# Kernel tuning notes

Hardware: AMD Instinct MI355X
Metric: run time of the kernel (lower is better)

The kernel has to match this reference:

```python
import jax, jax.numpy as jnp
import numpy as np

UP = 4  # upsample factor of DispUpsampleBySlantedPlane


def _l1_warp_cost(fea_l, fea_r, disp):
    """Warp fea_r horizontally by disp (grid_sample bilinear, zeros padding,
    align_corners=True) and return per-pixel L1 distance over channels.
    fea_l, fea_r: [B, C, H, W]; disp: [B, H, W] -> returns [B, H, W]."""
    B, C, H, W = fea_l.shape
    x = jnp.arange(W, dtype=disp.dtype)
    xf = x[None, None, :] - disp              # sample position in right image
    x0 = jnp.floor(xf)
    w1 = xf - x0                              # weight for x0+1
    w0 = 1.0 - w1
    x0i = x0.astype(jnp.int32)
    x1i = x0i + 1
    v0 = ((x0i >= 0) & (x0i < W)).astype(fea_l.dtype)  # zeros padding masks
    v1 = ((x1i >= 0) & (x1i < W)).astype(fea_l.dtype)
    x0c = jnp.clip(x0i, 0, W - 1)
    x1c = jnp.clip(x1i, 0, W - 1)
    idx0 = jnp.broadcast_to(x0c[:, None, :, :], (B, C, H, W))
    idx1 = jnp.broadcast_to(x1c[:, None, :, :], (B, C, H, W))
    g0 = jnp.take_along_axis(fea_r, idx0, axis=3)
    g1 = jnp.take_along_axis(fea_r, idx1, axis=3)
    warped = g0 * (w0 * v0)[:, None] + g1 * (w1 * v1)[:, None]
    return jnp.sum(jnp.abs(fea_l - warped), axis=1)  # L1 over channels


def _tile_warping(tile_plane, fea_l, fea_r):
    B, C, H, W = fea_l.shape
    h, w = tile_plane.shape[2], tile_plane.shape[3]
    d = tile_plane[:, 0]   # [B, h, w]
    dx = tile_plane[:, 1]
    dy = tile_plane[:, 2]
    # slanted-plane offsets for the 4x4 sub-pixels, centered at (UP-1)/2 = 1.5
    off = jnp.arange(UP, dtype=fea_l.dtype) - (UP - 1) / 2.0
    outs = []
    for disp_d in (-1.0, 0.0, 1.0):
        # disp0[b, di, dj, th, tw] = (d + disp_d) + off[di]*dy + off[dj]*dx
        disp0 = ((d + disp_d)[:, None, None]
                 + off[None, :, None, None, None] * dy[:, None, None]
                 + off[None, None, :, None, None] * dx[:, None, None])
        # PixelShuffle(4): full-res disparity [B, H, W]
        disp_full = disp0.transpose(0, 3, 1, 4, 2).reshape(B, H, W)
        cv = _l1_warp_cost(fea_l, fea_r, disp_full)        # [B, H, W]
        # cv[:, :, i::4, j::4] for i,j in 0..3, concatenated on channel dim
        local = cv.reshape(B, h, UP, w, UP).transpose(0, 2, 4, 1, 3)
        outs.append(local.reshape(B, UP * UP, h, w))       # [B, 16, h, w]
    return jnp.concatenate(outs, axis=1)                   # [B, 48, h, w]


def setup_inputs() -> dict:
    key = jax.random.key(0)
    k1, k2, k3 = jax.random.split(key, 3)
    B, C, H, W = 4, 16, 512, 960
    h, w = H // UP, W // UP
    tile_plane = jax.random.normal(k1, (B, 3, h, w), dtype=jnp.float32)
    fea_l = jax.random.normal(k2, (B, C, H, W), dtype=jnp.float32)
    fea_r = jax.random.normal(k3, (B, C, H, W), dtype=jnp.float32)
    return {"tile_plane": tile_plane, "fea_l": fea_l, "fea_r": fea_r}


def reference(tile_plane, fea_l, fea_r):
    return _tile_warping(tile_plane, fea_l, fea_r)
```

## Files before the change

### kernel.cpp

```cpp
#include <hip/hip_runtime.h>


#define NB 4
#define NC 16
#define NH 512
#define NW 960
#define TH 128
#define TW 240
#define HW (NH * NW)
#define SEG 256
#define GUARD 16
#define WIN (SEG + 2 * GUARD)
#define SLOTS (NC * WIN / 4)
#define SLOTS_PER_CH (WIN / 4)

typedef const __attribute__((address_space(1))) unsigned int* gas_u32;
typedef __attribute__((address_space(3))) unsigned int* las_u32;

__device__ __forceinline__ void stage16(const float* g, float* l) {
    __builtin_amdgcn_global_load_lds((gas_u32)g, (las_u32)l, 16, 0, 0);
}

__global__ __launch_bounds__(256, 8) void tile_warp_kernel(
    const float* __restrict__ tp,
    const float* __restrict__ fl,
    const float* __restrict__ fr,
    float* __restrict__ out)
{
    const int t = threadIdx.x;
    const int s = blockIdx.x;
    const int Y = blockIdx.y;
    const int b = blockIdx.z;
    const int base = s * SEG;
    const int X = base + t;

    __shared__ float lds[NC * WIN];

    const float* frrow = fr + (size_t)(b * NC) * HW + (size_t)Y * NW;

#pragma unroll
    for (int k = 0; k < 4; ++k) {
        const int slot = t + 256 * k;
        const int c = slot / SLOTS_PER_CH;
        const int off = slot - c * SLOTS_PER_CH;
        int gx = base - GUARD + 4 * off;
        gx = min(max(gx, 0), NW - 4);
        stage16(frrow + (size_t)c * HW + gx, &lds[4 * slot]);
    }
    if (t < SLOTS - 1024) {
        const int slot = t + 1024;
        const int c = slot / SLOTS_PER_CH;
        const int off = slot - c * SLOTS_PER_CH;
        int gx = base - GUARD + 4 * off;
        gx = min(max(gx, 0), NW - 4);
        stage16(frrow + (size_t)c * HW + gx, &lds[4 * slot]);
    }

    const int y = Y >> 2, i = Y & 3;
    const int j = X & 3;
    const int T = X >> 2;
    const int Tc = min(T, TW - 1);

    const int tpb = (b * 3 * TH + y) * TW + Tc;
    const float d   = tp[tpb];
    const float dxv = tp[tpb + TH * TW];
    const float dyv = tp[tpb + 2 * TH * TW];
    const float disp = d + ((float)i - 1.5f) * dyv + ((float)j - 1.5f) * dxv;
    const float xf  = (float)X - disp;
    const float x0f = floorf(xf);
    const float w1  = xf - x0f;
    const float w0  = 1.0f - w1;
    const int   x0  = (int)x0f;
    const int   p   = x0 - 1;
    const int   q   = p - base + GUARD;
    const int   qc  = min(max(q, 0), WIN - 4);
    const bool  spill = (q != qc) && (X < NW);

    float w0k[3], w1k[3];
#pragma unroll
    for (int kk = 0; kk < 3; ++kk) {
        const int xa = p + 2 - kk;
        const int xb = xa + 1;
        w0k[kk] = (xa >= 0 && xa < NW) ? w0 : 0.0f;
        w1k[kk] = (xb >= 0 && xb < NW) ? w1 : 0.0f;
    }

    const float* flp = fl + (size_t)(b * NC) * HW + (size_t)Y * NW + min(X, NW - 1);

    __syncthreads();

    float a0 = 0.f, a1 = 0.f, a2 = 0.f;
#pragma unroll
    for (int g = 0; g < 4; ++g) {
        float flv[4];
#pragma unroll
        for (int cc = 0; cc < 4; ++cc) flv[cc] = flp[(size_t)(4 * g + cc) * HW];
#pragma unroll
        for (int cc = 0; cc < 4; ++cc) {
            const float* L = &lds[(4 * g + cc) * WIN + qc];
            const float m0 = L[0], m1 = L[1], m2 = L[2], m3 = L[3];
            a0 += fabsf(flv[cc] - (m2 * w0k[0] + m3 * w1k[0]));
            a1 += fabsf(flv[cc] - (m1 * w0k[1] + m2 * w1k[1]));
            a2 += fabsf(flv[cc] - (m0 * w0k[2] + m1 * w1k[2]));
        }
    }

    if (__builtin_expect(spill, 0)) {
        a0 = a1 = a2 = 0.f;
        const int t0 = min(max(p,     0), NW - 1);
        const int t1 = min(max(p + 1, 0), NW - 1);
        const int t2 = min(max(p + 2, 0), NW - 1);
        const int t3 = min(max(p + 3, 0), NW - 1);
        for (int c = 0; c < NC; ++c) {
            const float* R = frrow + (size_t)c * HW;
            const float m0 = R[t0], m1 = R[t1], m2 = R[t2], m3 = R[t3];
            const float fv = flp[(size_t)c * HW];
            a0 += fabsf(fv - (m2 * w0k[0] + m3 * w1k[0]));
            a1 += fabsf(fv - (m1 * w0k[1] + m2 * w1k[1]));
            a2 += fabsf(fv - (m0 * w0k[2] + m1 * w1k[2]));
        }
    }

    if (X < NW) {
        const size_t ob = ((size_t)(b * 48 + i * 4 + j) * TH + y) * TW + T;
        out[ob]                        = a0;
        out[ob + 16 * (size_t)TH * TW] = a1;
        out[ob + 32 * (size_t)TH * TW] = a2;
    }
}

extern "C" void kernel_launch(void* const* d_in, const int* in_sizes, int n_in,
                              void* d_out, int out_size, void* d_ws, size_t ws_size,
                              hipStream_t stream) {
    const float* tp = (const float*)d_in[0];
    const float* fl = (const float*)d_in[1];
    const float* fr = (const float*)d_in[2];
    float* out = (float*)d_out;

    dim3 grid(4, NH, NB);
    dim3 block(256);
    tile_warp_kernel<<<grid, block, 0, stream>>>(tp, fl, fr, out);
}
```

Baseline: 274.2 us.

## Drop LDS staging of right features and gather directly from global memory

Removes the global_load_lds staging of a guarded right-feature window into shared memory, the barrier and the spill fallback path. Each thread now gathers its four right-feature taps per channel straight from global memory and relies on the cache. Blocks grow to 320 threads across 3 segments so the width of 960 divides evenly and the bounds checks go away. This trades LDS traffic and synchronisation for more global load instructions, with locality left to the L1/L2 caches.

```diff
diff --git a/kernel.cpp b/kernel.cpp
--- a/kernel.cpp
+++ b/kernel.cpp
@@ -8,20 +8,8 @@
 #define TH 128
 #define TW 240
 #define HW (NH * NW)
-#define SEG 256
-#define GUARD 16
-#define WIN (SEG + 2 * GUARD)
-#define SLOTS (NC * WIN / 4)
-#define SLOTS_PER_CH (WIN / 4)
 
-typedef const __attribute__((address_space(1))) unsigned int* gas_u32;
-typedef __attribute__((address_space(3))) unsigned int* las_u32;
-
-__device__ __forceinline__ void stage16(const float* g, float* l) {
-    __builtin_amdgcn_global_load_lds((gas_u32)g, (las_u32)l, 16, 0, 0);
-}
-
-__global__ __launch_bounds__(256, 8) void tile_warp_kernel(
+__global__ __launch_bounds__(320) void tile_warp_kernel(
     const float* __restrict__ tp,
     const float* __restrict__ fl,
     const float* __restrict__ fr,
@@ -31,37 +19,11 @@
     const int s = blockIdx.x;
     const int Y = blockIdx.y;
     const int b = blockIdx.z;
-    const int base = s * SEG;
-    const int X = base + t;
+    const int X = s * 320 + t;
+    const int y = Y >> 2, i = Y & 3;
+    const int j = X & 3, T = X >> 2;
 
-    __shared__ float lds[NC * WIN];
-
-    const float* frrow = fr + (size_t)(b * NC) * HW + (size_t)Y * NW;
-
-#pragma unroll
-    for (int k = 0; k < 4; ++k) {
-        const int slot = t + 256 * k;
-        const int c = slot / SLOTS_PER_CH;
-        const int off = slot - c * SLOTS_PER_CH;
-        int gx = base - GUARD + 4 * off;
-        gx = min(max(gx, 0), NW - 4);
-        stage16(frrow + (size_t)c * HW + gx, &lds[4 * slot]);
-    }
-    if (t < SLOTS - 1024) {
-        const int slot = t + 1024;
-        const int c = slot / SLOTS_PER_CH;
-        const int off = slot - c * SLOTS_PER_CH;
-        int gx = base - GUARD + 4 * off;
-        gx = min(max(gx, 0), NW - 4);
-        stage16(frrow + (size_t)c * HW + gx, &lds[4 * slot]);
-    }
-
-    const int y = Y >> 2, i = Y & 3;
-    const int j = X & 3;
-    const int T = X >> 2;
-    const int Tc = min(T, TW - 1);
-
-    const int tpb = (b * 3 * TH + y) * TW + Tc;
+    const int tpb = (b * 3 * TH + y) * TW + T;
     const float d   = tp[tpb];
     const float dxv = tp[tpb + TH * TW];
     const float dyv = tp[tpb + 2 * TH * TW];
@@ -70,11 +32,12 @@
     const float x0f = floorf(xf);
     const float w1  = xf - x0f;
     const float w0  = 1.0f - w1;
-    const int   x0  = (int)x0f;
-    const int   p   = x0 - 1;
-    const int   q   = p - base + GUARD;
-    const int   qc  = min(max(q, 0), WIN - 4);
-    const bool  spill = (q != qc) && (X < NW);
+    const int   p   = (int)x0f - 1;
+
+    const int t0 = min(max(p,     0), NW - 1);
+    const int t1 = min(max(p + 1, 0), NW - 1);
+    const int t2 = min(max(p + 2, 0), NW - 1);
+    const int t3 = min(max(p + 3, 0), NW - 1);
 
     float w0k[3], w1k[3];
 #pragma unroll
@@ -85,48 +48,27 @@
         w1k[kk] = (xb >= 0 && xb < NW) ? w1 : 0.0f;
     }
 
-    const float* flp = fl + (size_t)(b * NC) * HW + (size_t)Y * NW + min(X, NW - 1);
-
-    __syncthreads();
+    const float* frr = fr + (size_t)(b * NC) * HW + (size_t)Y * NW;
+    const float* flr = fl + (size_t)(b * NC) * HW + (size_t)Y * NW + X;
 
     float a0 = 0.f, a1 = 0.f, a2 = 0.f;
 #pragma unroll
-    for (int g = 0; g < 4; ++g) {
-        float flv[4];
-#pragma unroll
-        for (int cc = 0; cc < 4; ++cc) flv[cc] = flp[(size_t)(4 * g + cc) * HW];
-#pragma unroll
-        for (int cc = 0; cc < 4; ++cc) {
-            const float* L = &lds[(4 * g + cc) * WIN + qc];
-            const float m0 = L[0], m1 = L[1], m2 = L[2], m3 = L[3];
-            a0 += fabsf(flv[cc] - (m2 * w0k[0] + m3 * w1k[0]));
-            a1 += fabsf(flv[cc] - (m1 * w0k[1] + m2 * w1k[1]));
-            a2 += fabsf(flv[cc] - (m0 * w0k[2] + m1 * w1k[2]));
-        }
+    for (int c = 0; c < NC; ++c) {
+        const float* R = frr + (size_t)c * HW;
+        const float m0 = R[t0];
+        const float m1 = R[t1];
+        const float m2 = R[t2];
+        const float m3 = R[t3];
+        const float fv = flr[(size_t)c * HW];
+        a0 += fabsf(fv - (m2 * w0k[0] + m3 * w1k[0]));
+        a1 += fabsf(fv - (m1 * w0k[1] + m2 * w1k[1]));
+        a2 += fabsf(fv - (m0 * w0k[2] + m1 * w1k[2]));
     }
 
-    if (__builtin_expect(spill, 0)) {
-        a0 = a1 = a2 = 0.f;
-        const int t0 = min(max(p,     0), NW - 1);
-        const int t1 = min(max(p + 1, 0), NW - 1);
-        const int t2 = min(max(p + 2, 0), NW - 1);
-        const int t3 = min(max(p + 3, 0), NW - 1);
-        for (int c = 0; c < NC; ++c) {
-            const float* R = frrow + (size_t)c * HW;
-            const float m0 = R[t0], m1 = R[t1], m2 = R[t2], m3 = R[t3];
-            const float fv = flp[(size_t)c * HW];
-            a0 += fabsf(fv - (m2 * w0k[0] + m3 * w1k[0]));
-            a1 += fabsf(fv - (m1 * w0k[1] + m2 * w1k[1]));
-            a2 += fabsf(fv - (m0 * w0k[2] + m1 * w1k[2]));
-        }
-    }
-
-    if (X < NW) {
-        const size_t ob = ((size_t)(b * 48 + i * 4 + j) * TH + y) * TW + T;
-        out[ob]                        = a0;
-        out[ob + 16 * (size_t)TH * TW] = a1;
-        out[ob + 32 * (size_t)TH * TW] = a2;
-    }
+    const size_t ob = ((size_t)(b * 48 + i * 4 + j) * TH + y) * TW + T;
+    out[ob]                        = a0;
+    out[ob + 16 * (size_t)TH * TW] = a1;
+    out[ob + 32 * (size_t)TH * TW] = a2;
 }
 
 extern "C" void kernel_launch(void* const* d_in, const int* in_sizes, int n_in,
@@ -137,7 +79,7 @@
     const float* fr = (const float*)d_in[2];
     float* out = (float*)d_out;
 
-    dim3 grid(4, NH, NB);
-    dim3 block(256);
+    dim3 grid(3, NH, NB);
+    dim3 block(320);
     tile_warp_kernel<<<grid, block, 0, stream>>>(tp, fl, fr, out);
 }
```

After: 303.1 us. 10.6% more time.
